# Optimization experiments

Hardware: AMD Instinct MI355X
Metric: run time of the kernel (lower is better)

## Reference

```python
import jax, jax.numpy as jnp
import numpy as np

K = 16          # neighbors per query (args.k)
EPS_NORM = 1e-5  # LayerNorm / BatchNorm eps (torch default)


def _knn_edges(xyz, B, n):
    # batch-aware kNN: equal-sized batches, edges never cross batch boundary
    x = xyz.reshape(B, n, 3)
    d2 = jnp.sum((x[:, :, None, :] - x[:, None, :, :]) ** 2, -1)   # [B,n,n]
    _, idx = jax.lax.top_k(-d2, K)                                 # [B,n,K] local neighbor ids
    col = (idx + (jnp.arange(B) * n)[:, None, None]).reshape(-1)   # source (neighbor) [E]
    row = jnp.repeat(jnp.arange(B * n), K)                         # target (query)    [E]
    return row, col


def _forward(support_xyz, batch_index, features, lang_features, mask_flattened,
             W1, b1, ln_g, ln_b, W2, b2,
             Wl1, bl1, bn_g, bn_b, Wl2, bl2,
             Wr1, br1, Wr2, br2, row, col):
    N = support_xyz.shape[0]
    B, L, Fl = lang_features.shape
    # feat_encoder: Linear -> LayerNorm -> ReLU -> Linear
    h = features @ W1 + b1
    mu = h.mean(-1, keepdims=True)
    var = ((h - mu) ** 2).mean(-1, keepdims=True)
    h = (h - mu) / jnp.sqrt(var + EPS_NORM) * ln_g + ln_b
    feats = jax.nn.relu(h) @ W2 + b2                               # [N,F]
    # lang_encoder: Linear -> BatchNorm1d (batch statistics) -> ReLU -> Linear
    hl = lang_features.reshape(B * L, Fl) @ Wl1 + bl1
    mul = hl.mean(0)
    varl = ((hl - mul) ** 2).mean(0)
    hl = (hl - mul) / jnp.sqrt(varl + EPS_NORM) * bn_g + bn_b
    lang = (jax.nn.relu(hl) @ Wl2 + bl2).reshape(B, L, -1)         # [B,L,F]
    lang_flat = lang[batch_index]                                  # [N,L,F]
    # per-point / per-token attention logits
    atten = jnp.einsum('nf,nlf->nl', feats, lang_flat)             # [N,L]
    # segment softmax over incoming kNN edges (CenterOp max / add)
    attenmax = jax.ops.segment_max(atten[col], row, num_segments=N, indices_are_sorted=True)
    a = jnp.exp(atten[col] - attenmax[row])                        # [E,L]
    attensum = jax.ops.segment_sum(a, row, num_segments=N, indices_are_sorted=True)
    # CenterConv message
    att = a / attensum[row] * mask_flattened[row]                  # [E,L]
    att = att / (att.sum(-1, keepdims=True) + 1e-7)
    ctx = jnp.einsum('el,elf->ef', att, lang_flat[col])            # [E,F] attended lang feat
    xi, xj = support_xyz[row], support_xyz[col]
    d = xi - xj
    nrm = jnp.sqrt(jnp.sum(d * d, -1, keepdims=True) + 1e-12)
    ew = jnp.concatenate([xi, xj, d, nrm], -1)                     # [E,10]
    ew = jax.nn.relu(ew @ Wr1 + br1) @ Wr2 + br2                   # [E,F] rel_encoder
    msg = feats[col] * ctx * ew                                    # [E,F]
    rel = jax.ops.segment_sum(msg, row, num_segments=N, indices_are_sorted=True)
    return feats + rel


def setup_inputs() -> dict:
    key = jax.random.key(0)
    ks = jax.random.split(key, 12)
    B, n, L = 4, 1024, 16
    N = B * n
    Fv, Fl, F = 256, 768, 128
    def w(k, shp, fan):
        return jax.random.normal(k, shp, jnp.float32) / np.sqrt(fan).astype(np.float32)
    mask = (jax.random.uniform(ks[3], (N, L)) < 0.8).astype(jnp.float32).at[:, 0].set(1.0)
    return {
        'support_xyz': jax.random.normal(ks[0], (N, 3), jnp.float32),
        'batch_index': jnp.repeat(jnp.arange(B), n),
        'features': jax.random.normal(ks[1], (N, Fv), jnp.float32),
        'lang_features': jax.random.normal(ks[2], (B, L, Fl), jnp.float32),
        'mask_flattened': mask,
        'W1': w(ks[4], (Fv, F), Fv), 'b1': jnp.zeros(F, jnp.float32),
        'ln_g': jnp.ones(F, jnp.float32), 'ln_b': jnp.zeros(F, jnp.float32),
        'W2': w(ks[5], (F, F), F), 'b2': jnp.zeros(F, jnp.float32),
        'Wl1': w(ks[6], (Fl, F), Fl), 'bl1': jnp.zeros(F, jnp.float32),
        'bn_g': jnp.ones(F, jnp.float32), 'bn_b': jnp.zeros(F, jnp.float32),
        'Wl2': w(ks[7], (F, F), F), 'bl2': jnp.zeros(F, jnp.float32),
        'Wr1': w(ks[8], (10, 64), 10), 'br1': jnp.zeros(64, jnp.float32),
        'Wr2': w(ks[9], (64, F), 64), 'br2': jnp.zeros(F, jnp.float32),
    }


def reference(support_xyz, batch_index, features, lang_features, mask_flattened,
              W1, b1, ln_g, ln_b, W2, b2,
              Wl1, bl1, bn_g, bn_b, Wl2, bl2,
              Wr1, br1, Wr2, br2):
    B = lang_features.shape[0]
    n = support_xyz.shape[0] // B
    row, col = _knn_edges(support_xyz, B, n)
    return _forward(support_xyz, batch_index, features, lang_features, mask_flattened,
                    W1, b1, ln_g, ln_b, W2, b2,
                    Wl1, bl1, bn_g, bn_b, Wl2, bl2,
                    Wr1, br1, Wr2, br2, row, col)
```

## Files before the change

### kernel.cpp

```cpp
#include <hip/hip_runtime.h>

typedef unsigned long long u64;
typedef unsigned int u32;
typedef short short8 __attribute__((ext_vector_type(8)));
typedef float f32x4 __attribute__((ext_vector_type(4)));
typedef u32 u32x4v __attribute__((ext_vector_type(4)));

#define N_PTS   4096
#define B_SZ    4
#define L_TOK   16
#define FV      256
#define FL      768
#define FDIM    128
#define KNN     16
#define RH      64

#define MFMA_BF16(a, b, c) __builtin_amdgcn_mfma_f32_16x16x32_bf16((a), (b), (c), 0, 0, 0)

__device__ __forceinline__ short f2bf(float f) {
    unsigned int x = __float_as_uint(f);
    unsigned int r = (x + 0x7fffu + ((x >> 16) & 1u)) >> 16;
    return (short)r;
}

__device__ __forceinline__ u32 splitf(float f) {
    u32 bits = __float_as_uint(f);
    u32 hi = bits >> 16;
    float lof = f - __uint_as_float(bits & 0xffff0000u);
    u32 lo = __float_as_uint(lof) >> 16;
    return (hi << 16) | lo;
}

__global__ __launch_bounds__(256) void prep_kernel(const float* __restrict__ lf,
                                                   const float* __restrict__ Wl1,
                                                   const float* __restrict__ bl1,
                                                   const float* __restrict__ W1,
                                                   const float* __restrict__ W2,
                                                   const float* __restrict__ Wr2,
                                                   float* __restrict__ hl,
                                                   short* __restrict__ w1p_hi,
                                                   short* __restrict__ w1p_lo,
                                                   short* __restrict__ w2p_hi,
                                                   short* __restrict__ w2p_lo,
                                                   short* __restrict__ w2pe) {
    __shared__ float smem[1024];
    int b = blockIdx.x, t = threadIdx.x;
    int wid = t >> 6, lane = t & 63;
    int e = lane & 15, q = lane >> 4;

    if (b < 64) {
        int r = b;
        float* lrow = smem;
        float* part = smem + 768;
        for (int k = t; k < FL; k += 256) lrow[k] = lf[r * FL + k];
        __syncthreads();
        int c = t & 127, kh = t >> 7;
        float acc = (kh == 0) ? bl1[c] : 0.f;
        int k0 = kh * 384;
        for (int k = k0; k < k0 + 384; k++) acc += lrow[k] * Wl1[k * FDIM + c];
        part[kh * FDIM + c] = acc;
        __syncthreads();
        if (kh == 0) hl[r * FDIM + c] = part[c] + part[FDIM + c];
    } else if (b < 76) {
        int isW2 = (b >= 72);
        int ks = isW2 ? (b - 72) : (b - 64);
        const float* W = isW2 ? W2 : W1;
        short* ph = isW2 ? w2p_hi : w1p_hi;
        short* pl = isW2 ? w2p_lo : w1p_lo;
#pragma unroll
        for (int p = 0; p < 2; p++) {
            int ct = wid * 2 + p;
            short8 hi, lo;
#pragma unroll
            for (int j = 0; j < 8; j++) {
                u32 pr = splitf(W[(ks * 32 + q * 8 + j) * FDIM + ct * 16 + e]);
                hi[j] = (short)(pr >> 16);
                lo[j] = (short)(pr & 0xffffu);
            }
            int o = ((ks * 8 + ct) * 64 + lane) * 8;
            *(short8*)(ph + o) = hi;
            *(short8*)(pl + o) = lo;
        }
    } else {
        int ks = b - 76;
#pragma unroll
        for (int p = 0; p < 2; p++) {
            int ct = wid * 2 + p;
            short8 v;
#pragma unroll
            for (int j = 0; j < 8; j++)
                v[j] = f2bf(Wr2[(ks * 32 + q * 8 + j) * FDIM + ct * 16 + e]);
            *(short8*)(w2pe + ((ks * 8 + ct) * 64 + lane) * 8) = v;
        }
    }
}

__global__ __launch_bounds__(256) void k2_kernel(const float* __restrict__ features,
                                                 const short* __restrict__ w1p_hi,
                                                 const short* __restrict__ w1p_lo,
                                                 const short* __restrict__ w2p_hi,
                                                 const short* __restrict__ w2p_lo,
                                                 const float* __restrict__ b1,
                                                 const float* __restrict__ ln_g,
                                                 const float* __restrict__ ln_b,
                                                 const float* __restrict__ b2,
                                                 const float* __restrict__ hl,
                                                 const float* __restrict__ bn_g,
                                                 const float* __restrict__ bn_b,
                                                 const float* __restrict__ Wl2,
                                                 const float* __restrict__ bl2,
                                                 float* __restrict__ feats,
                                                 float* __restrict__ lang) {
    __shared__ u32 smem_u[8448];
    int b = blockIdx.x, t = threadIdx.x;
    int wid = t >> 6, lane = t & 63;
    int e = lane & 15, q = lane >> 4;
    if (b < 64) {
        int rt = b * 4 + wid;
        f32x4 acc[8];
#pragma unroll
        for (int ct = 0; ct < 8; ct++) {
            float v = b1[ct * 16 + e];
            acc[ct] = (f32x4){v, v, v, v};
        }
        for (int ks = 0; ks < 8; ks++) {
            const float* src = features + (rt * 16 + e) * FV + ks * 32 + q * 8;
            float4 f0 = *(const float4*)src;
            float4 f1 = *(const float4*)(src + 4);
            float av[8] = {f0.x, f0.y, f0.z, f0.w, f1.x, f1.y, f1.z, f1.w};
            short8 ah, al;
#pragma unroll
            for (int j = 0; j < 8; j++) {
                u32 pr = splitf(av[j]);
                ah[j] = (short)(pr >> 16);
                al[j] = (short)(pr & 0xffffu);
            }
#pragma unroll
            for (int ct = 0; ct < 8; ct++) {
                int bo = ((ks * 8 + ct) * 64 + lane) * 8;
                short8 bh = *(const short8*)(w1p_hi + bo);
                short8 bl = *(const short8*)(w1p_lo + bo);
                acc[ct] = MFMA_BF16(ah, bh, acc[ct]);
                acc[ct] = MFMA_BF16(al, bh, acc[ct]);
                acc[ct] = MFMA_BF16(ah, bl, acc[ct]);
            }
        }
        float s[4], sq[4];
#pragma unroll
        for (int r = 0; r < 4; r++) { s[r] = 0.f; sq[r] = 0.f; }
#pragma unroll
        for (int ct = 0; ct < 8; ct++)
#pragma unroll
            for (int r = 0; r < 4; r++) {
                float v = acc[ct][r];
                s[r] += v; sq[r] += v * v;
            }
#pragma unroll
        for (int off = 1; off < 16; off <<= 1)
#pragma unroll
            for (int r = 0; r < 4; r++) {
                s[r] += __shfl_xor(s[r], off, 16);
                sq[r] += __shfl_xor(sq[r], off, 16);
            }
        float mu[4], rs[4];
#pragma unroll
        for (int r = 0; r < 4; r++) {
            mu[r] = s[r] * (1.f / 128.f);
            float var = sq[r] * (1.f / 128.f) - mu[r] * mu[r];
            rs[r] = rsqrtf(var + 1e-5f);
        }
        u32* hrow = smem_u + wid * (16 * 132);
#pragma unroll
        for (int ct = 0; ct < 8; ct++) {
            float g = ln_g[ct * 16 + e], bb = ln_b[ct * 16 + e];
#pragma unroll
            for (int r = 0; r < 4; r++) {
                float n = fmaxf((acc[ct][r] - mu[r]) * rs[r] * g + bb, 0.f);
                hrow[(q * 4 + r) * 132 + ct * 16 + e] = splitf(n);
            }
        }
        f32x4 acc2[8];
#pragma unroll
        for (int ct = 0; ct < 8; ct++) {
            float v = b2[ct * 16 + e];
            acc2[ct] = (f32x4){v, v, v, v};
        }
#pragma unroll
        for (int ks = 0; ks < 4; ks++) {
            u32 hv[8];
            *(u32x4v*)&hv[0] = *(const u32x4v*)&hrow[e * 132 + ks * 32 + q * 8];
            *(u32x4v*)&hv[4] = *(const u32x4v*)&hrow[e * 132 + ks * 32 + q * 8 + 4];
            short8 ah, al;
#pragma unroll
            for (int j = 0; j < 8; j++) {
                ah[j] = (short)(hv[j] >> 16);
                al[j] = (short)(hv[j] & 0xffffu);
            }
#pragma unroll
            for (int ct = 0; ct < 8; ct++) {
                int bo = ((ks * 8 + ct) * 64 + lane) * 8;
                short8 bh = *(const short8*)(w2p_hi + bo);
                short8 bl = *(const short8*)(w2p_lo + bo);
                acc2[ct] = MFMA_BF16(ah, bh, acc2[ct]);
                acc2[ct] = MFMA_BF16(al, bh, acc2[ct]);
                acc2[ct] = MFMA_BF16(ah, bl, acc2[ct]);
            }
        }
#pragma unroll
        for (int ct = 0; ct < 8; ct++)
#pragma unroll
            for (int r = 0; r < 4; r++)
                feats[(rt * 16 + q * 4 + r) * FDIM + ct * 16 + e] = acc2[ct][r];
    } else {
        float* rl4 = (float*)smem_u;
        int tt = t & 127;
        int act = (t < 128);
        int r0 = (b - 64) * 4;
        if (act) {
            float s = 0.f, s2 = 0.f;
            for (int r = 0; r < 64; r++) {
                float v = hl[r * FDIM + tt];
                s += v; s2 += v * v;
            }
            float mu = s * (1.f / 64.f);
            float var = s2 * (1.f / 64.f) - mu * mu;
            float rs = rsqrtf(var + 1e-5f);
            float g = bn_g[tt], bb = bn_b[tt];
#pragma unroll
            for (int p = 0; p < 4; p++)
                rl4[p * FDIM + tt] = fmaxf((hl[(r0 + p) * FDIM + tt] - mu) * rs * g + bb, 0.f);
        }
        __syncthreads();
        if (act) {
            float bv = bl2[tt];
            float a0 = bv, a1 = bv, a2 = bv, a3 = bv;
            for (int k = 0; k < FDIM; k++) {
                float w = Wl2[k * FDIM + tt];
                a0 += rl4[0 * FDIM + k] * w;
                a1 += rl4[1 * FDIM + k] * w;
                a2 += rl4[2 * FDIM + k] * w;
                a3 += rl4[3 * FDIM + k] * w;
            }
            lang[(r0 + 0) * FDIM + tt] = a0;
            lang[(r0 + 1) * FDIM + tt] = a1;
            lang[(r0 + 2) * FDIM + tt] = a2;
            lang[(r0 + 3) * FDIM + tt] = a3;
        }
    }
}

__global__ __launch_bounds__(256) void atten_kernel(const float* __restrict__ feats,
                                                    const float* __restrict__ lang,
                                                    float* __restrict__ atten,
                                                    short* __restrict__ langp) {
    int b = blockIdx.x, t = threadIdx.x;
    int wid = t >> 6, lane = t & 63;
    int e = lane & 15, q = lane >> 4;
    if (b < 64) {
        int pt0 = (b * 4 + wid) * 16;
        int bi = pt0 >> 10;
        const float* arow = feats + (pt0 + e) * FDIM;
        const float* brow = lang + (bi * L_TOK + e) * FDIM;
        f32x4 acc = {0.f, 0.f, 0.f, 0.f};
#pragma unroll
        for (int ks = 0; ks < 4; ks++) {
            int off = ks * 32 + q * 8;
            float4 a0 = *(const float4*)(arow + off);
            float4 a1 = *(const float4*)(arow + off + 4);
            float4 c0 = *(const float4*)(brow + off);
            float4 c1 = *(const float4*)(brow + off + 4);
            float av[8] = {a0.x, a0.y, a0.z, a0.w, a1.x, a1.y, a1.z, a1.w};
            float bv[8] = {c0.x, c0.y, c0.z, c0.w, c1.x, c1.y, c1.z, c1.w};
            short8 ah, al, bh, bl;
#pragma unroll
            for (int j = 0; j < 8; j++) {
                u32 pa = splitf(av[j]);
                u32 pb = splitf(bv[j]);
                ah[j] = (short)(pa >> 16);
                al[j] = (short)(pa & 0xffffu);
                bh[j] = (short)(pb >> 16);
                bl[j] = (short)(pb & 0xffffu);
            }
            acc = MFMA_BF16(ah, bh, acc);
            acc = MFMA_BF16(al, bh, acc);
            acc = MFMA_BF16(ah, bl, acc);
        }
#pragma unroll
        for (int r = 0; r < 4; r++)
            atten[(pt0 + q * 4 + r) * L_TOK + e] = acc[r];
    } else {
        int bi = b - 64;
#pragma unroll
        for (int p = 0; p < 2; p++) {
            int tile = wid * 2 + p;
            short8 v;
            if (q < 2) {
#pragma unroll
                for (int j = 0; j < 8; j++)
                    v[j] = f2bf(lang[bi * L_TOK * FDIM + (q * 8 + j) * FDIM + tile * 16 + e]);
            } else {
#pragma unroll
                for (int j = 0; j < 8; j++) v[j] = 0;
            }
            *(short8*)(langp + ((bi * 8 + tile) * 64 + lane) * 8) = v;
        }
    }
}

__global__ __launch_bounds__(256) void knn_edge_kernel(const float* __restrict__ xyz,
                                                       const float* __restrict__ mask,
                                                       const float* __restrict__ Wr1,
                                                       const float* __restrict__ br1,
                                                       const float* __restrict__ br2,
                                                       const short* __restrict__ w2pe,
                                                       const short* __restrict__ langp,
                                                       const float* __restrict__ feats,
                                                       const float* __restrict__ atten,
                                                       float* __restrict__ out) {
    __shared__ int nbrs[4][16];
    int t = threadIdx.x;
    int wid = t >> 6, lane = t & 63;
    int quad = lane >> 4, e16 = lane & 15;
    int i = blockIdx.x * 4 + wid;
    int bi = i >> 10;
    int base = bi << 10;

    {
        float qx = xyz[i * 3 + 0];
        float qy = xyz[i * 3 + 1];
        float qz = xyz[i * 3 + 2];
        double key[16];
#pragma unroll
        for (int m = 0; m < 16; m++) {
            int jl = lane + (m << 6);
            int j = base + jl;
            float dx = qx - xyz[j * 3 + 0];
            float dy = qy - xyz[j * 3 + 1];
            float dz = qz - xyz[j * 3 + 2];
            float d2 = __fadd_rn(__fadd_rn(__fmul_rn(dx, dx), __fmul_rn(dy, dy)),
                                 __fmul_rn(dz, dz));
            key[m] = (double)__float_as_uint(d2) * 1024.0 + (double)jl;
        }
#pragma unroll
        for (int k = 2; k <= 16; k <<= 1) {
#pragma unroll
            for (int jj = k >> 1; jj > 0; jj >>= 1) {
#pragma unroll
                for (int ii = 0; ii < 16; ii++) {
                    int l = ii ^ jj;
                    if (l > ii) {
                        double lo = fmin(key[ii], key[l]);
                        double hi = fmax(key[ii], key[l]);
                        bool asc = ((ii & k) == 0);
                        key[ii] = asc ? lo : hi;
                        key[l] = asc ? hi : lo;
                    }
                }
            }
        }
#pragma unroll
        for (int lvl = 1; lvl <= 32; lvl <<= 1) {
            double pk[16];
#pragma unroll
            for (int ii = 0; ii < 16; ii++) pk[ii] = __shfl_xor(key[15 - ii], lvl, 64);
#pragma unroll
            for (int ii = 0; ii < 16; ii++) key[ii] = fmin(key[ii], pk[ii]);
            if (lvl != 32) {
#pragma unroll
                for (int jj = 8; jj > 0; jj >>= 1) {
#pragma unroll
                    for (int ii = 0; ii < 16; ii++) {
                        int l = ii ^ jj;
                        if (l > ii) {
                            double lo = fmin(key[ii], key[l]);
                            double hi = fmax(key[ii], key[l]);
                            key[ii] = lo;
                            key[l] = hi;
                        }
                    }
                }
            }
        }
        if (lane == 0) {
            int idx[16];
#pragma unroll
            for (int ii = 0; ii < 16; ii++)
                idx[ii] = base + (int)(((u64)key[ii]) & 1023u);
#pragma unroll
            for (int w = 0; w < 4; w++) {
                int4 v = {idx[4 * w], idx[4 * w + 1], idx[4 * w + 2], idx[4 * w + 3]};
                *(int4*)&nbrs[wid][4 * w] = v;
            }
        }
    }
    int idxe = nbrs[wid][e16];
    int idxr[4];
#pragma unroll
    for (int r = 0; r < 4; r++) idxr[r] = nbrs[wid][quad * 4 + r];

    float sat[8];
    if (quad < 2) {
        const float4* ap = (const float4*)(atten + idxe * L_TOK + quad * 8);
        float4 a0 = ap[0], a1 = ap[1];
        sat[0] = a0.x; sat[1] = a0.y; sat[2] = a0.z; sat[3] = a0.w;
        sat[4] = a1.x; sat[5] = a1.y; sat[6] = a1.z; sat[7] = a1.w;
    } else {
#pragma unroll
        for (int j = 0; j < 8; j++) sat[j] = 0.f;
    }

    float mx[8];
#pragma unroll
    for (int j = 0; j < 8; j++) mx[j] = sat[j];
#pragma unroll
    for (int off = 1; off < 16; off <<= 1) {
#pragma unroll
        for (int j = 0; j < 8; j++) mx[j] = fmaxf(mx[j], __shfl_xor(mx[j], off, 16));
    }
    float ex[8], sm[8];
#pragma unroll
    for (int j = 0; j < 8; j++) { ex[j] = __expf(sat[j] - mx[j]); sm[j] = ex[j]; }
#pragma unroll
    for (int off = 1; off < 16; off <<= 1) {
#pragma unroll
        for (int j = 0; j < 8; j++) sm[j] += __shfl_xor(sm[j], off, 16);
    }
    float st[8];
    if (quad < 2) {
        const float4* mp = (const float4*)(mask + i * L_TOK + quad * 8);
        float4 m0 = mp[0], m1 = mp[1];
        float mv[8] = {m0.x, m0.y, m0.z, m0.w, m1.x, m1.y, m1.z, m1.w};
#pragma unroll
        for (int j = 0; j < 8; j++) st[j] = ex[j] * (mv[j] / sm[j]);
    } else {
#pragma unroll
        for (int j = 0; j < 8; j++) st[j] = 0.f;
    }
    float s = st[0] + st[1] + st[2] + st[3] + st[4] + st[5] + st[6] + st[7];
    s += __shfl_xor(s, 16, 64);
    s += __shfl_xor(s, 32, 64);
    float inv2 = 1.f / (s + 1e-7f);
    short8 sattA;
#pragma unroll
    for (int j = 0; j < 8; j++) sattA[j] = f2bf(st[j] * inv2);

    float xi0 = xyz[i * 3 + 0], xi1 = xyz[i * 3 + 1], xi2 = xyz[i * 3 + 2];
    float xj0 = xyz[idxe * 3 + 0], xj1 = xyz[idxe * 3 + 1], xj2 = xyz[idxe * 3 + 2];
    float d0 = xi0 - xj0, d1 = xi1 - xj1, d2v = xi2 - xj2;
    float nr = sqrtf(d0 * d0 + d1 * d1 + d2v * d2v + 1e-12f);
    float ein[10] = {xi0, xi1, xi2, xj0, xj1, xj2, d0, d1, d2v, nr};
    short8 hidA[2];
#pragma unroll
    for (int sstep = 0; sstep < 2; sstep++) {
        int k0 = sstep * 32 + quad * 8;
        float h[8];
        const float4* bp = (const float4*)(br1 + k0);
        float4 b0 = bp[0], b1v = bp[1];
        h[0] = b0.x; h[1] = b0.y; h[2] = b0.z; h[3] = b0.w;
        h[4] = b1v.x; h[5] = b1v.y; h[6] = b1v.z; h[7] = b1v.w;
#pragma unroll
        for (int m = 0; m < 10; m++) {
            const float4* wp = (const float4*)(Wr1 + m * RH + k0);
            float4 w0 = wp[0], w1 = wp[1];
            float em = ein[m];
            h[0] += em * w0.x; h[1] += em * w0.y; h[2] += em * w0.z; h[3] += em * w0.w;
            h[4] += em * w1.x; h[5] += em * w1.y; h[6] += em * w1.z; h[7] += em * w1.w;
        }
#pragma unroll
        for (int j = 0; j < 8; j++) hidA[sstep][j] = f2bf(fmaxf(h[j], 0.f));
    }

#pragma unroll 2
    for (int tile = 0; tile < 8; tile++) {
        int cc = tile * 16 + e16;
        f32x4 accew = {0.f, 0.f, 0.f, 0.f};
#pragma unroll
        for (int sstep = 0; sstep < 2; sstep++) {
            short8 w2B = *(const short8*)(w2pe + ((sstep * 8 + tile) * 64 + lane) * 8);
            accew = MFMA_BF16(hidA[sstep], w2B, accew);
        }
        short8 lsB = *(const short8*)(langp + ((bi * 8 + tile) * 64 + lane) * 8);
        f32x4 accctx = {0.f, 0.f, 0.f, 0.f};
        accctx = MFMA_BF16(sattA, lsB, accctx);

        float br2c = br2[cc];
        float msum = 0.f;
#pragma unroll
        for (int r = 0; r < 4; r++) {
            float fj = feats[idxr[r] * FDIM + cc];
            msum += fj * accctx[r] * (accew[r] + br2c);
        }
        msum += __shfl_xor(msum, 16, 64);
        msum += __shfl_xor(msum, 32, 64);
        if (lane < 16)
            out[i * FDIM + cc] = feats[i * FDIM + cc] + msum;
    }
}

extern "C" void kernel_launch(void* const* d_in, const int* in_sizes, int n_in,
                              void* d_out, int out_size, void* d_ws, size_t ws_size,
                              hipStream_t stream) {
    const float* xyz   = (const float*)d_in[0];
    const float* features = (const float*)d_in[2];
    const float* lang_f   = (const float*)d_in[3];
    const float* mask     = (const float*)d_in[4];
    const float* W1   = (const float*)d_in[5];
    const float* b1   = (const float*)d_in[6];
    const float* ln_g = (const float*)d_in[7];
    const float* ln_b = (const float*)d_in[8];
    const float* W2   = (const float*)d_in[9];
    const float* b2   = (const float*)d_in[10];
    const float* Wl1  = (const float*)d_in[11];
    const float* bl1  = (const float*)d_in[12];
    const float* bn_g = (const float*)d_in[13];
    const float* bn_b = (const float*)d_in[14];
    const float* Wl2  = (const float*)d_in[15];
    const float* bl2  = (const float*)d_in[16];
    const float* Wr1  = (const float*)d_in[17];
    const float* br1  = (const float*)d_in[18];
    const float* Wr2  = (const float*)d_in[19];
    const float* br2  = (const float*)d_in[20];

    float* ws_feats = (float*)d_ws;
    float* ws_atten = ws_feats + N_PTS * FDIM;
    float* ws_lang  = ws_atten + N_PTS * L_TOK;
    float* ws_hl    = ws_lang + B_SZ * L_TOK * FDIM;
    short* w1p_hi   = (short*)(ws_hl + 64 * FDIM);
    short* w1p_lo   = w1p_hi + FV * FDIM;
    short* w2p_hi   = w1p_lo + FV * FDIM;
    short* w2p_lo   = w2p_hi + FDIM * FDIM;
    short* w2pe     = w2p_lo + FDIM * FDIM;
    short* langp    = w2pe + RH * FDIM;

    prep_kernel<<<78, 256, 0, stream>>>(lang_f, Wl1, bl1, W1, W2, Wr2,
                                        ws_hl, w1p_hi, w1p_lo, w2p_hi, w2p_lo, w2pe);
    k2_kernel<<<80, 256, 0, stream>>>(features, w1p_hi, w1p_lo, w2p_hi, w2p_lo,
                                      b1, ln_g, ln_b, b2,
                                      ws_hl, bn_g, bn_b, Wl2, bl2,
                                      ws_feats, ws_lang);
    atten_kernel<<<68, 256, 0, stream>>>(ws_feats, ws_lang, ws_atten, langp);
    knn_edge_kernel<<<N_PTS / 4, 256, 0, stream>>>(xyz, mask, Wr1, br1, br2,
                                                   w2pe, langp, ws_feats, ws_atten,
                                                   (float*)d_out);
}
```

Measured before the change: 171.2 us.

## Move kNN into mid kernel and compute attention logits inside edge kernel

The kNN bitonic selection moves from the edge kernel into the feature-encoder kernel as extra blocks, so it runs alongside the feature and language GEMMs. The separate atten and langp pack kernel is removed. Each edge wave now computes the attention logits for its 16 neighbors directly with MFMA, and packs lang to bf16 on the fly. This drops one launch and the atten/langp round trips through memory. In exchange, logits are recomputed per edge rather than per point (16x more attention MFMA work), neighbor indices go through global memory, and the lang bf16 conversion is repeated in every tile iteration.

```diff
diff --git a/kernel.cpp b/kernel.cpp
--- a/kernel.cpp
+++ b/kernel.cpp
@@ -95,28 +95,100 @@
     }
 }
 
-__global__ __launch_bounds__(256) void k2_kernel(const float* __restrict__ features,
-                                                 const short* __restrict__ w1p_hi,
-                                                 const short* __restrict__ w1p_lo,
-                                                 const short* __restrict__ w2p_hi,
-                                                 const short* __restrict__ w2p_lo,
-                                                 const float* __restrict__ b1,
-                                                 const float* __restrict__ ln_g,
-                                                 const float* __restrict__ ln_b,
-                                                 const float* __restrict__ b2,
-                                                 const float* __restrict__ hl,
-                                                 const float* __restrict__ bn_g,
-                                                 const float* __restrict__ bn_b,
-                                                 const float* __restrict__ Wl2,
-                                                 const float* __restrict__ bl2,
-                                                 float* __restrict__ feats,
-                                                 float* __restrict__ lang) {
+__global__ __launch_bounds__(256) void mid_kernel(const float* __restrict__ xyz,
+                                                  const float* __restrict__ features,
+                                                  const short* __restrict__ w1p_hi,
+                                                  const short* __restrict__ w1p_lo,
+                                                  const short* __restrict__ w2p_hi,
+                                                  const short* __restrict__ w2p_lo,
+                                                  const float* __restrict__ b1,
+                                                  const float* __restrict__ ln_g,
+                                                  const float* __restrict__ ln_b,
+                                                  const float* __restrict__ b2,
+                                                  const float* __restrict__ hl,
+                                                  const float* __restrict__ bn_g,
+                                                  const float* __restrict__ bn_b,
+                                                  const float* __restrict__ Wl2,
+                                                  const float* __restrict__ bl2,
+                                                  int* __restrict__ knn,
+                                                  float* __restrict__ feats,
+                                                  float* __restrict__ lang) {
     __shared__ u32 smem_u[8448];
     int b = blockIdx.x, t = threadIdx.x;
     int wid = t >> 6, lane = t & 63;
     int e = lane & 15, q = lane >> 4;
-    if (b < 64) {
-        int rt = b * 4 + wid;
+
+    if (b < 1024) {
+        int qi = b * 4 + wid;
+        int base = (qi >> 10) << 10;
+        float qx = xyz[qi * 3 + 0];
+        float qy = xyz[qi * 3 + 1];
+        float qz = xyz[qi * 3 + 2];
+        double key[16];
+#pragma unroll
+        for (int m = 0; m < 16; m++) {
+            int jl = lane + (m << 6);
+            int j = base + jl;
+            float dx = qx - xyz[j * 3 + 0];
+            float dy = qy - xyz[j * 3 + 1];
+            float dz = qz - xyz[j * 3 + 2];
+            float d2 = __fadd_rn(__fadd_rn(__fmul_rn(dx, dx), __fmul_rn(dy, dy)),
+                                 __fmul_rn(dz, dz));
+            key[m] = (double)__float_as_uint(d2) * 1024.0 + (double)jl;
+        }
+#pragma unroll
+        for (int k = 2; k <= 16; k <<= 1) {
+#pragma unroll
+            for (int jj = k >> 1; jj > 0; jj >>= 1) {
+#pragma unroll
+                for (int ii = 0; ii < 16; ii++) {
+                    int l = ii ^ jj;
+                    if (l > ii) {
+                        double lo = fmin(key[ii], key[l]);
+                        double hi = fmax(key[ii], key[l]);
+                        bool asc = ((ii & k) == 0);
+                        key[ii] = asc ? lo : hi;
+                        key[l] = asc ? hi : lo;
+                    }
+                }
+            }
+        }
+#pragma unroll
+        for (int lvl = 1; lvl <= 32; lvl <<= 1) {
+            double pk[16];
+#pragma unroll
+            for (int ii = 0; ii < 16; ii++) pk[ii] = __shfl_xor(key[15 - ii], lvl, 64);
+#pragma unroll
+            for (int ii = 0; ii < 16; ii++) key[ii] = fmin(key[ii], pk[ii]);
+            if (lvl != 32) {
+#pragma unroll
+                for (int jj = 8; jj > 0; jj >>= 1) {
+#pragma unroll
+                    for (int ii = 0; ii < 16; ii++) {
+                        int l = ii ^ jj;
+                        if (l > ii) {
+                            double lo = fmin(key[ii], key[l]);
+                            double hi = fmax(key[ii], key[l]);
+                            key[ii] = lo;
+                            key[l] = hi;
+                        }
+                    }
+                }
+            }
+        }
+        if (lane == 0) {
+            int idx[16];
+#pragma unroll
+            for (int ii = 0; ii < 16; ii++)
+                idx[ii] = base + (int)(((u64)key[ii]) & 1023u);
+#pragma unroll
+            for (int w = 0; w < 4; w++) {
+                int4 v = {idx[4 * w], idx[4 * w + 1], idx[4 * w + 2], idx[4 * w + 3]};
+                *(int4*)&knn[qi * KNN + 4 * w] = v;
+            }
+        }
+    } else if (b < 1088) {
+        int rt = (b - 1024) * 4 + wid;
         f32x4 acc[8];
 #pragma unroll
         for (int ct = 0; ct < 8; ct++) {
@@ -215,7 +287,7 @@
         float* rl4 = (float*)smem_u;
         int tt = t & 127;
         int act = (t < 128);
-        int r0 = (b - 64) * 4;
+        int r0 = (b - 1088) * 4;
         if (act) {
             float s = 0.f, s2 = 0.f;
             for (int r = 0; r < 64; r++) {
@@ -249,200 +321,89 @@
     }
 }
 
-__global__ __launch_bounds__(256) void atten_kernel(const float* __restrict__ feats,
-                                                    const float* __restrict__ lang,
-                                                    float* __restrict__ atten,
-                                                    short* __restrict__ langp) {
-    int b = blockIdx.x, t = threadIdx.x;
-    int wid = t >> 6, lane = t & 63;
-    int e = lane & 15, q = lane >> 4;
-    if (b < 64) {
-        int pt0 = (b * 4 + wid) * 16;
-        int bi = pt0 >> 10;
-        const float* arow = feats + (pt0 + e) * FDIM;
-        const float* brow = lang + (bi * L_TOK + e) * FDIM;
-        f32x4 acc = {0.f, 0.f, 0.f, 0.f};
-#pragma unroll
-        for (int ks = 0; ks < 4; ks++) {
-            int off = ks * 32 + q * 8;
-            float4 a0 = *(const float4*)(arow + off);
-            float4 a1 = *(const float4*)(arow + off + 4);
-            float4 c0 = *(const float4*)(brow + off);
-            float4 c1 = *(const float4*)(brow + off + 4);
-            float av[8] = {a0.x, a0.y, a0.z, a0.w, a1.x, a1.y, a1.z, a1.w};
-            float bv[8] = {c0.x, c0.y, c0.z, c0.w, c1.x, c1.y, c1.z, c1.w};
-            short8 ah, al, bh, bl;
-#pragma unroll
-            for (int j = 0; j < 8; j++) {
-                u32 pa = splitf(av[j]);
-                u32 pb = splitf(bv[j]);
-                ah[j] = (short)(pa >> 16);
-                al[j] = (short)(pa & 0xffffu);
-                bh[j] = (short)(pb >> 16);
-                bl[j] = (short)(pb & 0xffffu);
-            }
-            acc = MFMA_BF16(ah, bh, acc);
-            acc = MFMA_BF16(al, bh, acc);
-            acc = MFMA_BF16(ah, bl, acc);
-        }
-#pragma unroll
-        for (int r = 0; r < 4; r++)
-            atten[(pt0 + q * 4 + r) * L_TOK + e] = acc[r];
-    } else {
-        int bi = b - 64;
-#pragma unroll
-        for (int p = 0; p < 2; p++) {
-            int tile = wid * 2 + p;
-            short8 v;
-            if (q < 2) {
-#pragma unroll
-                for (int j = 0; j < 8; j++)
-                    v[j] = f2bf(lang[bi * L_TOK * FDIM + (q * 8 + j) * FDIM + tile * 16 + e]);
-            } else {
-#pragma unroll
-                for (int j = 0; j < 8; j++) v[j] = 0;
-            }
-            *(short8*)(langp + ((bi * 8 + tile) * 64 + lane) * 8) = v;
-        }
-    }
-}
-
-__global__ __launch_bounds__(256) void knn_edge_kernel(const float* __restrict__ xyz,
-                                                       const float* __restrict__ mask,
-                                                       const float* __restrict__ Wr1,
-                                                       const float* __restrict__ br1,
-                                                       const float* __restrict__ br2,
-                                                       const short* __restrict__ w2pe,
-                                                       const short* __restrict__ langp,
-                                                       const float* __restrict__ feats,
-                                                       const float* __restrict__ atten,
-                                                       float* __restrict__ out) {
-    __shared__ int nbrs[4][16];
+__global__ __launch_bounds__(256) void edge_kernel(const float* __restrict__ xyz,
+                                                   const float* __restrict__ mask,
+                                                   const float* __restrict__ Wr1,
+                                                   const float* __restrict__ br1,
+                                                   const float* __restrict__ br2,
+                                                   const int* __restrict__ knn,
+                                                   const short* __restrict__ w2pe,
+                                                   const float* __restrict__ lang,
+                                                   const float* __restrict__ feats,
+                                                   float* __restrict__ out) {
+    __shared__ float att_t[4][16][17];
     int t = threadIdx.x;
     int wid = t >> 6, lane = t & 63;
     int quad = lane >> 4, e16 = lane & 15;
     int i = blockIdx.x * 4 + wid;
     int bi = i >> 10;
-    int base = bi << 10;
-
-    {
-        float qx = xyz[i * 3 + 0];
-        float qy = xyz[i * 3 + 1];
-        float qz = xyz[i * 3 + 2];
-        double key[16];
-#pragma unroll
-        for (int m = 0; m < 16; m++) {
-            int jl = lane + (m << 6);
-            int j = base + jl;
-            float dx = qx - xyz[j * 3 + 0];
-            float dy = qy - xyz[j * 3 + 1];
-            float dz = qz - xyz[j * 3 + 2];
-            float d2 = __fadd_rn(__fadd_rn(__fmul_rn(dx, dx), __fmul_rn(dy, dy)),
-                                 __fmul_rn(dz, dz));
-            key[m] = (double)__float_as_uint(d2) * 1024.0 + (double)jl;
-        }
-#pragma unroll
-        for (int k = 2; k <= 16; k <<= 1) {
-#pragma unroll
-            for (int jj = k >> 1; jj > 0; jj >>= 1) {
-#pragma unroll
-                for (int ii = 0; ii < 16; ii++) {
-                    int l = ii ^ jj;
-                    if (l > ii) {
-                        double lo = fmin(key[ii], key[l]);
-                        double hi = fmax(key[ii], key[l]);
-                        bool asc = ((ii & k) == 0);
-                        key[ii] = asc ? lo : hi;
-                        key[l] = asc ? hi : lo;
-                    }
-                }
-            }
-        }
-#pragma unroll
-        for (int lvl = 1; lvl <= 32; lvl <<= 1) {
-            double pk[16];
-#pragma unroll
-            for (int ii = 0; ii < 16; ii++) pk[ii] = __shfl_xor(key[15 - ii], lvl, 64);
-#pragma unroll
-            for (int ii = 0; ii < 16; ii++) key[ii] = fmin(key[ii], pk[ii]);
-            if (lvl != 32) {
-#pragma unroll
-                for (int jj = 8; jj > 0; jj >>= 1) {
-#pragma unroll
-                    for (int ii = 0; ii < 16; ii++) {
-                        int l = ii ^ jj;
-                        if (l > ii) {
-                            double lo = fmin(key[ii], key[l]);
-                            double hi = fmax(key[ii], key[l]);
-                            key[ii] = lo;
-                            key[l] = hi;
-                        }
-                    }
-                }
-            }
-        }
-        if (lane == 0) {
-            int idx[16];
-#pragma unroll
-            for (int ii = 0; ii < 16; ii++)
-                idx[ii] = base + (int)(((u64)key[ii]) & 1023u);
-#pragma unroll
-            for (int w = 0; w < 4; w++) {
-                int4 v = {idx[4 * w], idx[4 * w + 1], idx[4 * w + 2], idx[4 * w + 3]};
-                *(int4*)&nbrs[wid][4 * w] = v;
-            }
-        }
+
+    int idxe = knn[i * KNN + e16];
+    int idxr[4];
+#pragma unroll
+    for (int r = 0; r < 4; r++) idxr[r] = knn[i * KNN + quad * 4 + r];
+
+    const float* arow = feats + idxe * FDIM;
+    const float* brow = lang + (bi * L_TOK + e16) * FDIM;
+    f32x4 acc = {0.f, 0.f, 0.f, 0.f};
+#pragma unroll
+    for (int ks = 0; ks < 4; ks++) {
+        int off = ks * 32 + quad * 8;
+        float4 a0 = *(const float4*)(arow + off);
+        float4 a1 = *(const float4*)(arow + off + 4);
+        float4 c0 = *(const float4*)(brow + off);
+        float4 c1 = *(const float4*)(brow + off + 4);
+        float av[8] = {a0.x, a0.y, a0.z, a0.w, a1.x, a1.y, a1.z, a1.w};
+        float bv[8] = {c0.x, c0.y, c0.z, c0.w, c1.x, c1.y, c1.z, c1.w};
+        short8 ah, al, bh, bl;
+#pragma unroll
+        for (int j = 0; j < 8; j++) {
+            u32 pa = splitf(av[j]);
+            u32 pb = splitf(bv[j]);
+            ah[j] = (short)(pa >> 16);
+            al[j] = (short)(pa & 0xffffu);
+            bh[j] = (short)(pb >> 16);
+            bl[j] = (short)(pb & 0xffffu);
+        }
+        acc = MFMA_BF16(ah, bh, acc);
+        acc = MFMA_BF16(al, bh, acc);
+        acc = MFMA_BF16(ah, bl, acc);
     }
-    int idxe = nbrs[wid][e16];
-    int idxr[4];
-#pragma unroll
-    for (int r = 0; r < 4; r++) idxr[r] = nbrs[wid][quad * 4 + r];
-
-    float sat[8];
+
+    float mx = fmaxf(fmaxf(acc[0], acc[1]), fmaxf(acc[2], acc[3]));
+    mx = fmaxf(mx, __shfl_xor(mx, 16, 64));
+    mx = fmaxf(mx, __shfl_xor(mx, 32, 64));
+    float ex[4];
+    float sm = 0.f;
+#pragma unroll
+    for (int r = 0; r < 4; r++) { ex[r] = __expf(acc[r] - mx); sm += ex[r]; }
+    sm += __shfl_xor(sm, 16, 64);
+    sm += __shfl_xor(sm, 32, 64);
+    float mv = mask[i * L_TOK + e16];
+    float st[4];
+#pragma unroll
+    for (int r = 0; r < 4; r++) st[r] = ex[r] * (mv / sm);
+    float sn[4];
+#pragma unroll
+    for (int r = 0; r < 4; r++) sn[r] = st[r];
+#pragma unroll
+    for (int off = 1; off < 16; off <<= 1)
+#pragma unroll
+        for (int r = 0; r < 4; r++) sn[r] += __shfl_xor(sn[r], off, 16);
+    float attf[4];
+#pragma unroll
+    for (int r = 0; r < 4; r++) attf[r] = st[r] * (1.f / (sn[r] + 1e-7f));
+
+#pragma unroll
+    for (int r = 0; r < 4; r++) att_t[wid][quad * 4 + r][e16] = attf[r];
+    short8 sattA;
     if (quad < 2) {
-        const float4* ap = (const float4*)(atten + idxe * L_TOK + quad * 8);
-        float4 a0 = ap[0], a1 = ap[1];
-        sat[0] = a0.x; sat[1] = a0.y; sat[2] = a0.z; sat[3] = a0.w;
-        sat[4] = a1.x; sat[5] = a1.y; sat[6] = a1.z; sat[7] = a1.w;
+#pragma unroll
+        for (int j = 0; j < 8; j++) sattA[j] = f2bf(att_t[wid][e16][quad * 8 + j]);
     } else {
 #pragma unroll
-        for (int j = 0; j < 8; j++) sat[j] = 0.f;
+        for (int j = 0; j < 8; j++) sattA[j] = 0;
     }
-
-    float mx[8];
-#pragma unroll
-    for (int j = 0; j < 8; j++) mx[j] = sat[j];
-#pragma unroll
-    for (int off = 1; off < 16; off <<= 1) {
-#pragma unroll
-        for (int j = 0; j < 8; j++) mx[j] = fmaxf(mx[j], __shfl_xor(mx[j], off, 16));
-    }
-    float ex[8], sm[8];
-#pragma unroll
-    for (int j = 0; j < 8; j++) { ex[j] = __expf(sat[j] - mx[j]); sm[j] = ex[j]; }
-#pragma unroll
-    for (int off = 1; off < 16; off <<= 1) {
-#pragma unroll
-        for (int j = 0; j < 8; j++) sm[j] += __shfl_xor(sm[j], off, 16);
-    }
-    float st[8];
-    if (quad < 2) {
-        const float4* mp = (const float4*)(mask + i * L_TOK + quad * 8);
-        float4 m0 = mp[0], m1 = mp[1];
-        float mv[8] = {m0.x, m0.y, m0.z, m0.w, m1.x, m1.y, m1.z, m1.w};
-#pragma unroll
-        for (int j = 0; j < 8; j++) st[j] = ex[j] * (mv[j] / sm[j]);
-    } else {
-#pragma unroll
-        for (int j = 0; j < 8; j++) st[j] = 0.f;
-    }
-    float s = st[0] + st[1] + st[2] + st[3] + st[4] + st[5] + st[6] + st[7];
-    s += __shfl_xor(s, 16, 64);
-    s += __shfl_xor(s, 32, 64);
-    float inv2 = 1.f / (s + 1e-7f);
-    short8 sattA;
-#pragma unroll
-    for (int j = 0; j < 8; j++) sattA[j] = f2bf(st[j] * inv2);
 
     float xi0 = xyz[i * 3 + 0], xi1 = xyz[i * 3 + 1], xi2 = xyz[i * 3 + 2];
     float xj0 = xyz[idxe * 3 + 0], xj1 = xyz[idxe * 3 + 1], xj2 = xyz[idxe * 3 + 2];
@@ -479,7 +440,15 @@
             short8 w2B = *(const short8*)(w2pe + ((sstep * 8 + tile) * 64 + lane) * 8);
             accew = MFMA_BF16(hidA[sstep], w2B, accew);
         }
-        short8 lsB = *(const short8*)(langp + ((bi * 8 + tile) * 64 + lane) * 8);
+        short8 lsB;
+        if (quad < 2) {
+#pragma unroll
+            for (int j = 0; j < 8; j++)
+                lsB[j] = f2bf(lang[bi * L_TOK * FDIM + (quad * 8 + j) * FDIM + cc]);
+        } else {
+#pragma unroll
+            for (int j = 0; j < 8; j++) lsB[j] = 0;
+        }
         f32x4 accctx = {0.f, 0.f, 0.f, 0.f};
         accctx = MFMA_BF16(sattA, lsB, accctx);
 
@@ -522,24 +491,23 @@
     const float* br2  = (const float*)d_in[20];
 
     float* ws_feats = (float*)d_ws;
-    float* ws_atten = ws_feats + N_PTS * FDIM;
-    float* ws_lang  = ws_atten + N_PTS * L_TOK;
+    float* ws_lang  = ws_feats + N_PTS * FDIM;
     float* ws_hl    = ws_lang + B_SZ * L_TOK * FDIM;
-    short* w1p_hi   = (short*)(ws_hl + 64 * FDIM);
+    int*   ws_knn   = (int*)(ws_hl + 64 * FDIM);
+    short* w1p_hi   = (short*)(ws_knn + N_PTS * KNN);
     short* w1p_lo   = w1p_hi + FV * FDIM;
     short* w2p_hi   = w1p_lo + FV * FDIM;
     short* w2p_lo   = w2p_hi + FDIM * FDIM;
     short* w2pe     = w2p_lo + FDIM * FDIM;
-    short* langp    = w2pe + RH * FDIM;
 
     prep_kernel<<<78, 256, 0, stream>>>(lang_f, Wl1, bl1, W1, W2, Wr2,
                                         ws_hl, w1p_hi, w1p_lo, w2p_hi, w2p_lo, w2pe);
-    k2_kernel<<<80, 256, 0, stream>>>(features, w1p_hi, w1p_lo, w2p_hi, w2p_lo,
-                                      b1, ln_g, ln_b, b2,
-                                      ws_hl, bn_g, bn_b, Wl2, bl2,
-                                      ws_feats, ws_lang);
-    atten_kernel<<<68, 256, 0, stream>>>(ws_feats, ws_lang, ws_atten, langp);
-    knn_edge_kernel<<<N_PTS / 4, 256, 0, stream>>>(xyz, mask, Wr1, br1, br2,
-                                                   w2pe, langp, ws_feats, ws_atten,
-                                                   (float*)d_out);
+    mid_kernel<<<1104, 256, 0, stream>>>(xyz, features,
+                                         w1p_hi, w1p_lo, w2p_hi, w2p_lo,
+                                         b1, ln_g, ln_b, b2,
+                                         ws_hl, bn_g, bn_b, Wl2, bl2,
+                                         ws_knn, ws_feats, ws_lang);
+    edge_kernel<<<N_PTS / 4, 256, 0, stream>>>(xyz, mask, Wr1, br1, br2,
+                                               ws_knn, w2pe, ws_lang, ws_feats,
+                                               (float*)d_out);
 }
```

New measurement: 165.4 us. 1.03x faster.
